# Kernel optimization log

Measured on AMD Instinct MI355X. Metric: run time of the kernel, lower is better.

Reference implementation:

```python
import jax, jax.numpy as jnp
import numpy as np

B, U, D_DEC, D_ENC = 32, 4096, 512, 512
ATT_UNITS, NUM_HEADS = 512, 4
HEAD_DIM = ATT_UNITS // NUM_HEADS
CONV_FILTERS, CONV_K = 32, 31
INIT = 0.075


def setup_inputs() -> dict:
    key = jax.random.key(0)
    ks = jax.random.split(key, 12)
    u = lambda k, shape: jax.random.uniform(k, shape, jnp.float32, -INIT, INIT)
    return {
        "dec_state": jax.random.normal(ks[0], (B, D_DEC), jnp.float32),
        "enc_state": jax.random.normal(ks[1], (B, U, D_ENC), jnp.float32),
        "prev_attention_weights": jax.random.uniform(ks[2], (B, U), jnp.float32),
        # stacked per-head Dense params
        "Wphi": u(ks[3], (NUM_HEADS, D_DEC, HEAD_DIM)),
        "bphi": jnp.zeros((NUM_HEADS, HEAD_DIM), jnp.float32),
        "Wpsi": u(ks[4], (NUM_HEADS, D_ENC, HEAD_DIM)),
        "bpsi": jnp.zeros((NUM_HEADS, HEAD_DIM), jnp.float32),
        # Conv1D kernel in WIO layout: (kernel_size, in_ch=1, out_ch=32), no bias
        "conv_kernel": jax.random.uniform(ks[5], (CONV_K, 1, CONV_FILTERS), jnp.float32, -0.1, 0.1),
        "Wloc": u(ks[6], (CONV_FILTERS, NUM_HEADS)),
        "Wout": u(ks[7], (NUM_HEADS * D_ENC, ATT_UNITS)),
        "bout": jnp.zeros((ATT_UNITS,), jnp.float32),
    }


def reference(dec_state, enc_state, prev_attention_weights,
              Wphi, bphi, Wpsi, bpsi, conv_kernel, Wloc, Wout, bout):
    # location features: Conv1D(same, no bias) over prev attention weights
    loc_feat = jax.lax.conv_general_dilated(
        prev_attention_weights[:, :, None], conv_kernel,
        window_strides=(1,), padding="SAME",
        dimension_numbers=("NWC", "WIO", "NWC"))            # (B, U, 32)
    loc_bias = loc_feat @ Wloc                                 # (B, U, H)
    loc_bias = jnp.transpose(loc_bias, (0, 2, 1))              # (B, H, U)

    # batched per-head projections (replaces the Python per-head loop)
    phi_s = jnp.einsum("bd,hdk->bhk", dec_state, Wphi) + bphi          # (B, H, hd)
    psi_h = jnp.einsum("bue,hek->bhuk", enc_state, Wpsi) + bpsi[:, None, :]  # (B, H, U, hd)

    energy = jnp.einsum("bhk,bhuk->bhu", phi_s, psi_h) + loc_bias      # (B, H, U)
    attn = jax.nn.softmax(energy, axis=-1)                              # (B, H, U)

    context = jnp.einsum("bhu,bue->bhe", attn, enc_state)               # (B, H, E)
    combined = context.reshape(context.shape[0], -1)                    # (B, H*E)
    context_vector = combined @ Wout + bout                             # (B, ATT_UNITS)
    attention_weights = jnp.mean(attn, axis=1)                          # (B, U)
    return context_vector, attention_weights
```

## Files before the change

kernel.cpp:

```cpp
#include <hip/hip_runtime.h>
#include <math.h>

#define B  32
#define U  4096
#define D  512
#define H  4
#define HD 128
#define CK 31
#define CF 32
#define AU 512

#define BPB    32
#define ROWS_W 32

static __device__ __forceinline__ float readlane_f(float v, int l) {
    return __int_as_float(__builtin_amdgcn_readlane(__float_as_int(v), l));
}

__global__ __launch_bounds__(256) void prep_kernel(
    const float* __restrict__ dec,
    const float* __restrict__ Wphi,
    const float* __restrict__ bphi,
    const float* __restrict__ Wpsi,
    const float* __restrict__ bpsi,
    const float* __restrict__ convk,
    const float* __restrict__ Wloc,
    float* __restrict__ ws_v,
    float* __restrict__ ws_const,
    float* __restrict__ ws_ck)
{
    __shared__ float decs[D];
    __shared__ float phis2[2][HD];
    __shared__ float phis[HD];
    const int b = blockIdx.x / H, h = blockIdx.x % H;
    const int tid = threadIdx.x;

    for (int i = tid; i < D; i += 256) decs[i] = dec[b * D + i];
    __syncthreads();

    {
        const int k = tid & 127, half = tid >> 7;
        const int d0 = half * 256;
        float acc = 0.f;
        const float* wp = Wphi + (size_t)h * D * HD + (size_t)d0 * HD + k;
        #pragma unroll 8
        for (int d = 0; d < 256; ++d) acc += decs[d0 + d] * wp[(size_t)d * HD];
        phis2[half][k] = acc;
    }
    __syncthreads();
    if (tid < HD) phis[tid] = phis2[0][tid] + phis2[1][tid] + bphi[h * HD + tid];
    __syncthreads();

    if (tid == 0) {
        float c = 0.f;
        for (int k = 0; k < HD; ++k) c += phis[k] * bpsi[h * HD + k];
        ws_const[b * H + h] = c;
    }

    for (int e = tid; e < D; e += 256) {
        const float* wq = Wpsi + ((size_t)h * D + e) * HD;
        float acc = 0.f;
        #pragma unroll 8
        for (int k = 0; k < HD; ++k) acc += wq[k] * phis[k];
        ws_v[((size_t)b * H + h) * D + e] = acc;
    }

    if (blockIdx.x == 0 && tid < CK * H) {
        int t = tid / H, hh = tid % H;
        float acc = 0.f;
        for (int f = 0; f < CF; ++f) acc += convk[t * CF + f] * Wloc[f * H + hh];
        ws_ck[t * H + hh] = acc;
    }
}

__global__ __launch_bounds__(256, 4) void fused_pass1(
    const float* __restrict__ enc,
    const float* __restrict__ prevw,
    const float* __restrict__ ws_v,
    const float* __restrict__ ws_const,
    const float* __restrict__ ws_ck,
    float* __restrict__ energy,
    float* __restrict__ pctx,
    float* __restrict__ pms)
{
    const int b    = blockIdx.y;
    const int blk  = blockIdx.x;
    const int tid  = threadIdx.x;
    const int lane = tid & 63;
    const int wave = tid >> 6;
    const int ubase = (blk * 4 + wave) * ROWS_W;

    __shared__ float lctx[4][H][D];
    __shared__ float lms[4][H][2];
    __shared__ float lalpha[H][4];

    float4 v0[H], v1[H];
    #pragma unroll
    for (int h = 0; h < H; ++h) {
        const float* vp = ws_v + ((size_t)b * H + h) * D + lane * 8;
        v0[h] = *(const float4*)vp;
        v1[h] = *(const float4*)(vp + 4);
    }
    float ckr[H] = {0.f, 0.f, 0.f, 0.f};
    if (lane < CK) {
        #pragma unroll
        for (int h = 0; h < H; ++h) ckr[h] = ws_ck[lane * H + h];
    }
    float ct[H];
    #pragma unroll
    for (int h = 0; h < H; ++h) ct[h] = ws_const[b * H + h];

    float w0;
    {
        const int gi = ubase - 15 + lane;
        w0 = (gi >= 0 && gi < U) ? prevw[b * U + gi] : 0.f;
    }

    float m0 = -3.402823466e38f, m1 = m0, m2 = m0, m3 = m0;
    float s0 = 0.f, s1 = 0.f, s2 = 0.f, s3 = 0.f;
    float4 z = {0.f, 0.f, 0.f, 0.f};
    float4 c00 = z, c01 = z, c10 = z, c11 = z, c20 = z, c21 = z, c30 = z, c31 = z;

    const bool b16 = (lane & 16) != 0;
    const bool b32 = (lane & 32) != 0;

    const float* encb = enc + ((size_t)b * U + ubase) * D + lane * 8;
    float4 e0 = *(const float4*)encb;
    float4 e1 = *(const float4*)(encb + 4);

    for (int r = 0; r < ROWS_W; ++r) {
        float4 n0, n1;
        if (r < ROWS_W - 1) {
            const float* nx = encb + (size_t)(r + 1) * D;
            n0 = *(const float4*)nx;
            n1 = *(const float4*)(nx + 4);
        }
        const int u = ubase + r;
        float pw = __int_as_float(
            __builtin_amdgcn_ds_bpermute((r + lane) << 2, __float_as_int(w0)));

        float p0 = pw * ckr[0]
            + e0.x*v0[0].x + e0.y*v0[0].y + e0.z*v0[0].z + e0.w*v0[0].w
            + e1.x*v1[0].x + e1.y*v1[0].y + e1.z*v1[0].z + e1.w*v1[0].w;
        float p1 = pw * ckr[1]
            + e0.x*v0[1].x + e0.y*v0[1].y + e0.z*v0[1].z + e0.w*v0[1].w
            + e1.x*v1[1].x + e1.y*v1[1].y + e1.z*v1[1].z + e1.w*v1[1].w;
        float p2 = pw * ckr[2]
            + e0.x*v0[2].x + e0.y*v0[2].y + e0.z*v0[2].z + e0.w*v0[2].w
            + e1.x*v1[2].x + e1.y*v1[2].y + e1.z*v1[2].z + e1.w*v1[2].w;
        float p3 = pw * ckr[3]
            + e0.x*v0[3].x + e0.y*v0[3].y + e0.z*v0[3].z + e0.w*v0[3].w
            + e1.x*v1[3].x + e1.y*v1[3].y + e1.z*v1[3].z + e1.w*v1[3].w;

        float keepA = b16 ? p1 : p0, sendA = b16 ? p0 : p1;
        float a  = keepA + __shfl_xor(sendA, 16);
        float keepB = b16 ? p3 : p2, sendB = b16 ? p2 : p3;
        float bb = keepB + __shfl_xor(sendB, 16);
        float keepC = b32 ? bb : a, sendC = b32 ? a : bb;
        float c = keepC + __shfl_xor(sendC, 32);
        c += __shfl_xor(c, 1);
        c += __shfl_xor(c, 2);
        c += __shfl_xor(c, 4);
        c += __shfl_xor(c, 8);
        float eh0 = readlane_f(c, 0)  + ct[0];
        float eh1 = readlane_f(c, 16) + ct[1];
        float eh2 = readlane_f(c, 32) + ct[2];
        float eh3 = readlane_f(c, 48) + ct[3];

        if (lane < H) {
            float ev = (lane == 0) ? eh0 : (lane == 1) ? eh1 : (lane == 2) ? eh2 : eh3;
            energy[((size_t)b * H + lane) * U + u] = ev;
        }

        float mn0 = fmaxf(m0, eh0), mn1 = fmaxf(m1, eh1);
        float mn2 = fmaxf(m2, eh2), mn3 = fmaxf(m3, eh3);
        if (mn0 > m0 || mn1 > m1 || mn2 > m2 || mn3 > m3) {
            float a0 = __expf(m0 - mn0), a1 = __expf(m1 - mn1);
            float a2 = __expf(m2 - mn2), a3 = __expf(m3 - mn3);
            s0 *= a0; s1 *= a1; s2 *= a2; s3 *= a3;
            c00.x*=a0; c00.y*=a0; c00.z*=a0; c00.w*=a0; c01.x*=a0; c01.y*=a0; c01.z*=a0; c01.w*=a0;
            c10.x*=a1; c10.y*=a1; c10.z*=a1; c10.w*=a1; c11.x*=a1; c11.y*=a1; c11.z*=a1; c11.w*=a1;
            c20.x*=a2; c20.y*=a2; c20.z*=a2; c20.w*=a2; c21.x*=a2; c21.y*=a2; c21.z*=a2; c21.w*=a2;
            c30.x*=a3; c30.y*=a3; c30.z*=a3; c30.w*=a3; c31.x*=a3; c31.y*=a3; c31.z*=a3; c31.w*=a3;
            m0 = mn0; m1 = mn1; m2 = mn2; m3 = mn3;
        }
        float w0e = __expf(eh0 - m0), w1e = __expf(eh1 - m1);
        float w2e = __expf(eh2 - m2), w3e = __expf(eh3 - m3);
        s0 += w0e; s1 += w1e; s2 += w2e; s3 += w3e;
        c00.x += w0e*e0.x; c00.y += w0e*e0.y; c00.z += w0e*e0.z; c00.w += w0e*e0.w;
        c01.x += w0e*e1.x; c01.y += w0e*e1.y; c01.z += w0e*e1.z; c01.w += w0e*e1.w;
        c10.x += w1e*e0.x; c10.y += w1e*e0.y; c10.z += w1e*e0.z; c10.w += w1e*e0.w;
        c11.x += w1e*e1.x; c11.y += w1e*e1.y; c11.z += w1e*e1.z; c11.w += w1e*e1.w;
        c20.x += w2e*e0.x; c20.y += w2e*e0.y; c20.z += w2e*e0.z; c20.w += w2e*e0.w;
        c21.x += w2e*e1.x; c21.y += w2e*e1.y; c21.z += w2e*e1.z; c21.w += w2e*e1.w;
        c30.x += w3e*e0.x; c30.y += w3e*e0.y; c30.z += w3e*e0.z; c30.w += w3e*e0.w;
        c31.x += w3e*e1.x; c31.y += w3e*e1.y; c31.z += w3e*e1.z; c31.w += w3e*e1.w;

        e0 = n0; e1 = n1;
    }

    *(float4*)&lctx[wave][0][lane * 8]     = c00;
    *(float4*)&lctx[wave][0][lane * 8 + 4] = c01;
    *(float4*)&lctx[wave][1][lane * 8]     = c10;
    *(float4*)&lctx[wave][1][lane * 8 + 4] = c11;
    *(float4*)&lctx[wave][2][lane * 8]     = c20;
    *(float4*)&lctx[wave][2][lane * 8 + 4] = c21;
    *(float4*)&lctx[wave][3][lane * 8]     = c30;
    *(float4*)&lctx[wave][3][lane * 8 + 4] = c31;
    if (lane == 0) {
        lms[wave][0][0] = m0; lms[wave][0][1] = s0;
        lms[wave][1][0] = m1; lms[wave][1][1] = s1;
        lms[wave][2][0] = m2; lms[wave][2][1] = s2;
        lms[wave][3][0] = m3; lms[wave][3][1] = s3;
    }
    __syncthreads();

    const size_t pbase = ((size_t)(b * BPB + blk)) * H;
    if (tid < H) {
        const int h = tid;
        float M = fmaxf(fmaxf(lms[0][h][0], lms[1][h][0]),
                        fmaxf(lms[2][h][0], lms[3][h][0]));
        float S = 0.f;
        #pragma unroll
        for (int w = 0; w < 4; ++w) {
            float al = __expf(lms[w][h][0] - M);
            lalpha[h][w] = al;
            S += al * lms[w][h][1];
        }
        pms[(pbase + h) * 2]     = M;
        pms[(pbase + h) * 2 + 1] = S;
    }
    __syncthreads();

    #pragma unroll
    for (int h = 0; h < H; ++h) {
        const float a0 = lalpha[h][0], a1 = lalpha[h][1];
        const float a2 = lalpha[h][2], a3 = lalpha[h][3];
        #pragma unroll
        for (int half = 0; half < 2; ++half) {
            const int d = tid + half * 256;
            float val = a0 * lctx[0][h][d] + a1 * lctx[1][h][d]
                      + a2 * lctx[2][h][d] + a3 * lctx[3][h][d];
            pctx[(pbase + h) * D + d] = val;
        }
    }
}

__global__ __launch_bounds__(256) void combine_kernel(
    const float* __restrict__ pctx,
    const float* __restrict__ pms,
    float* __restrict__ ctx,
    float* __restrict__ MS)
{
    const int bh = blockIdx.x;
    const int b = bh >> 2, h = bh & 3;
    const int tid = threadIdx.x;
    __shared__ float sm[BPB], ss[BPB], salpha[BPB];
    __shared__ float MSsh[2];

    if (tid < BPB) {
        sm[tid] = pms[(((size_t)b * BPB + tid) * H + h) * 2];
        ss[tid] = pms[(((size_t)b * BPB + tid) * H + h) * 2 + 1];
    }
    __syncthreads();
    if (tid == 0) {
        float M = -3.402823466e38f;
        for (int i = 0; i < BPB; ++i) M = fmaxf(M, sm[i]);
        float S = 0.f;
        for (int i = 0; i < BPB; ++i) {
            float al = __expf(sm[i] - M);
            salpha[i] = al;
            S += al * ss[i];
        }
        MSsh[0] = M; MSsh[1] = S;
        MS[bh * 2] = M; MS[bh * 2 + 1] = S;
    }
    __syncthreads();
    const float invS = 1.0f / MSsh[1];

    float acc0 = 0.f, acc1 = 0.f;
    const float* base = pctx + ((size_t)b * BPB * H + h) * D;
    #pragma unroll 4
    for (int i = 0; i < BPB; ++i) {
        float al = salpha[i];
        const float* p = base + (size_t)i * H * D;
        acc0 += al * p[tid];
        acc1 += al * p[tid + 256];
    }
    ctx[(size_t)bh * D + tid]       = acc0 * invS;
    ctx[(size_t)bh * D + tid + 256] = acc1 * invS;
}

__global__ __launch_bounds__(256) void attw_kernel(
    const float* __restrict__ energy,
    const float* __restrict__ MS,
    float* __restrict__ attw)
{
    const int b = blockIdx.x, tid = threadIdx.x;
    float M[H], iS[H];
    #pragma unroll
    for (int h = 0; h < H; ++h) {
        M[h]  = MS[(b * H + h) * 2];
        iS[h] = 1.0f / MS[(b * H + h) * 2 + 1];
    }
    #pragma unroll
    for (int i = 0; i < 16; ++i) {
        const int u = tid + i * 256;
        float acc = 0.f;
        #pragma unroll
        for (int h = 0; h < H; ++h)
            acc += __expf(energy[((size_t)b * H + h) * U + u] - M[h]) * iS[h];
        attw[(size_t)b * U + u] = acc * 0.25f;
    }
}

__global__ __launch_bounds__(256) void outproj_kernel(
    const float* __restrict__ ctx,
    const float* __restrict__ Wout,
    const float* __restrict__ bout,
    float* __restrict__ outv)
{
    const int b = blockIdx.y;
    const int j = blockIdx.x * 256 + threadIdx.x;
    const int i0 = blockIdx.z * 256;
    __shared__ float c_s[256];
    c_s[threadIdx.x] = ctx[(size_t)b * (H * D) + i0 + threadIdx.x];
    __syncthreads();

    float acc = (blockIdx.z == 0) ? bout[j] : 0.f;
    #pragma unroll 8
    for (int i = 0; i < 256; ++i)
        acc += c_s[i] * Wout[(size_t)(i0 + i) * AU + j];
    atomicAdd(&outv[(size_t)b * AU + j], acc);
}

extern "C" void kernel_launch(void* const* d_in, const int* in_sizes, int n_in,
                              void* d_out, int out_size, void* d_ws, size_t ws_size,
                              hipStream_t stream) {
    const float* dec   = (const float*)d_in[0];
    const float* enc   = (const float*)d_in[1];
    const float* prevw = (const float*)d_in[2];
    const float* Wphi  = (const float*)d_in[3];
    const float* bphi  = (const float*)d_in[4];
    const float* Wpsi  = (const float*)d_in[5];
    const float* bpsi  = (const float*)d_in[6];
    const float* convk = (const float*)d_in[7];
    const float* Wloc  = (const float*)d_in[8];
    const float* Wout  = (const float*)d_in[9];
    const float* bout  = (const float*)d_in[10];

    float* out  = (float*)d_out;
    float* outv = out;
    float* attw = out + B * AU;

    float* ws        = (float*)d_ws;
    float* ws_v      = ws;
    float* ws_const  = ws + 65536;
    float* ws_ck     = ws + 65664;
    float* ws_energy = ws + 65792;
    float* ws_pctx   = ws_energy + (size_t)B*H*U;
    float* ws_pms    = ws_pctx + (size_t)B*BPB*H*D;
    float* ws_MS     = ws_pms + (size_t)B*BPB*H*2;
    float* ws_ctx    = ws_MS + 256;

    hipMemsetAsync(outv, 0, (size_t)B * AU * sizeof(float), stream);

    prep_kernel<<<dim3(B * H), 256, 0, stream>>>(dec, Wphi, bphi, Wpsi, bpsi,
                                                 convk, Wloc, ws_v, ws_const, ws_ck);
    fused_pass1<<<dim3(BPB, B), 256, 0, stream>>>(enc, prevw, ws_v, ws_const,
                                                  ws_ck, ws_energy, ws_pctx, ws_pms);
    combine_kernel<<<dim3(B * H), 256, 0, stream>>>(ws_pctx, ws_pms, ws_ctx, ws_MS);
    attw_kernel<<<dim3(B), 256, 0, stream>>>(ws_energy, ws_MS, attw);
    outproj_kernel<<<dim3(2, B, 8), 256, 0, stream>>>(ws_ctx, Wout, bout, outv);
}
```

Baseline: 437.2 us.

## Deepen enc prefetch, batch energy stores per wave, widen attw grid

The fused pass now prefetches encoder rows two steps ahead instead of one and unrolls the row loop by two, so more memory latency is hidden. Energy values are collected in registers (lane r keeps row r) and written once after the loop as coalesced stores, replacing a scattered per-row store by four lanes. The attention-weight kernel grid grows from B to 8×B blocks, so many more CUs share the elementwise pass. These raise register pressure in the hot loop in exchange.

```diff
diff --git a/kernel.cpp b/kernel.cpp
--- a/kernel.cpp
+++ b/kernel.cpp
@@ -120,37 +120,40 @@
     float s0 = 0.f, s1 = 0.f, s2 = 0.f, s3 = 0.f;
     float4 z = {0.f, 0.f, 0.f, 0.f};
     float4 c00 = z, c01 = z, c10 = z, c11 = z, c20 = z, c21 = z, c30 = z, c31 = z;
+    float ea0 = 0.f, ea1 = 0.f, ea2 = 0.f, ea3 = 0.f;
 
     const bool b16 = (lane & 16) != 0;
     const bool b32 = (lane & 32) != 0;
 
     const float* encb = enc + ((size_t)b * U + ubase) * D + lane * 8;
-    float4 e0 = *(const float4*)encb;
-    float4 e1 = *(const float4*)(encb + 4);
-
+    float4 eA0 = *(const float4*)encb;
+    float4 eA1 = *(const float4*)(encb + 4);
+    float4 eB0 = *(const float4*)(encb + D);
+    float4 eB1 = *(const float4*)(encb + D + 4);
+
+    #pragma unroll 2
     for (int r = 0; r < ROWS_W; ++r) {
-        float4 n0, n1;
-        if (r < ROWS_W - 1) {
-            const float* nx = encb + (size_t)(r + 1) * D;
-            n0 = *(const float4*)nx;
-            n1 = *(const float4*)(nx + 4);
-        }
-        const int u = ubase + r;
+        float4 eC0, eC1;
+        if (r < ROWS_W - 2) {
+            const float* nx = encb + (size_t)(r + 2) * D;
+            eC0 = *(const float4*)nx;
+            eC1 = *(const float4*)(nx + 4);
+        }
         float pw = __int_as_float(
             __builtin_amdgcn_ds_bpermute((r + lane) << 2, __float_as_int(w0)));
 
         float p0 = pw * ckr[0]
-            + e0.x*v0[0].x + e0.y*v0[0].y + e0.z*v0[0].z + e0.w*v0[0].w
-            + e1.x*v1[0].x + e1.y*v1[0].y + e1.z*v1[0].z + e1.w*v1[0].w;
+            + eA0.x*v0[0].x + eA0.y*v0[0].y + eA0.z*v0[0].z + eA0.w*v0[0].w
+            + eA1.x*v1[0].x + eA1.y*v1[0].y + eA1.z*v1[0].z + eA1.w*v1[0].w;
         float p1 = pw * ckr[1]
-            + e0.x*v0[1].x + e0.y*v0[1].y + e0.z*v0[1].z + e0.w*v0[1].w
-            + e1.x*v1[1].x + e1.y*v1[1].y + e1.z*v1[1].z + e1.w*v1[1].w;
+            + eA0.x*v0[1].x + eA0.y*v0[1].y + eA0.z*v0[1].z + eA0.w*v0[1].w
+            + eA1.x*v1[1].x + eA1.y*v1[1].y + eA1.z*v1[1].z + eA1.w*v1[1].w;
         float p2 = pw * ckr[2]
-            + e0.x*v0[2].x + e0.y*v0[2].y + e0.z*v0[2].z + e0.w*v0[2].w
-            + e1.x*v1[2].x + e1.y*v1[2].y + e1.z*v1[2].z + e1.w*v1[2].w;
+            + eA0.x*v0[2].x + eA0.y*v0[2].y + eA0.z*v0[2].z + eA0.w*v0[2].w
+            + eA1.x*v1[2].x + eA1.y*v1[2].y + eA1.z*v1[2].z + eA1.w*v1[2].w;
         float p3 = pw * ckr[3]
-            + e0.x*v0[3].x + e0.y*v0[3].y + e0.z*v0[3].z + e0.w*v0[3].w
-            + e1.x*v1[3].x + e1.y*v1[3].y + e1.z*v1[3].z + e1.w*v1[3].w;
+            + eA0.x*v0[3].x + eA0.y*v0[3].y + eA0.z*v0[3].z + eA0.w*v0[3].w
+            + eA1.x*v1[3].x + eA1.y*v1[3].y + eA1.z*v1[3].z + eA1.w*v1[3].w;
 
         float keepA = b16 ? p1 : p0, sendA = b16 ? p0 : p1;
         float a  = keepA + __shfl_xor(sendA, 16);
@@ -167,10 +170,10 @@
         float eh2 = readlane_f(c, 32) + ct[2];
         float eh3 = readlane_f(c, 48) + ct[3];
 
-        if (lane < H) {
-            float ev = (lane == 0) ? eh0 : (lane == 1) ? eh1 : (lane == 2) ? eh2 : eh3;
-            energy[((size_t)b * H + lane) * U + u] = ev;
-        }
+        ea0 = (lane == r) ? eh0 : ea0;
+        ea1 = (lane == r) ? eh1 : ea1;
+        ea2 = (lane == r) ? eh2 : ea2;
+        ea3 = (lane == r) ? eh3 : ea3;
 
         float mn0 = fmaxf(m0, eh0), mn1 = fmaxf(m1, eh1);
         float mn2 = fmaxf(m2, eh2), mn3 = fmaxf(m3, eh3);
@@ -187,16 +190,25 @@
         float w0e = __expf(eh0 - m0), w1e = __expf(eh1 - m1);
         float w2e = __expf(eh2 - m2), w3e = __expf(eh3 - m3);
         s0 += w0e; s1 += w1e; s2 += w2e; s3 += w3e;
-        c00.x += w0e*e0.x; c00.y += w0e*e0.y; c00.z += w0e*e0.z; c00.w += w0e*e0.w;
-        c01.x += w0e*e1.x; c01.y += w0e*e1.y; c01.z += w0e*e1.z; c01.w += w0e*e1.w;
-        c10.x += w1e*e0.x; c10.y += w1e*e0.y; c10.z += w1e*e0.z; c10.w += w1e*e0.w;
-        c11.x += w1e*e1.x; c11.y += w1e*e1.y; c11.z += w1e*e1.z; c11.w += w1e*e1.w;
-        c20.x += w2e*e0.x; c20.y += w2e*e0.y; c20.z += w2e*e0.z; c20.w += w2e*e0.w;
-        c21.x += w2e*e1.x; c21.y += w2e*e1.y; c21.z += w2e*e1.z; c21.w += w2e*e1.w;
-        c30.x += w3e*e0.x; c30.y += w3e*e0.y; c30.z += w3e*e0.z; c30.w += w3e*e0.w;
-        c31.x += w3e*e1.x; c31.y += w3e*e1.y; c31.z += w3e*e1.z; c31.w += w3e*e1.w;
-
-        e0 = n0; e1 = n1;
+        c00.x += w0e*eA0.x; c00.y += w0e*eA0.y; c00.z += w0e*eA0.z; c00.w += w0e*eA0.w;
+        c01.x += w0e*eA1.x; c01.y += w0e*eA1.y; c01.z += w0e*eA1.z; c01.w += w0e*eA1.w;
+        c10.x += w1e*eA0.x; c10.y += w1e*eA0.y; c10.z += w1e*eA0.z; c10.w += w1e*eA0.w;
+        c11.x += w1e*eA1.x; c11.y += w1e*eA1.y; c11.z += w1e*eA1.z; c11.w += w1e*eA1.w;
+        c20.x += w2e*eA0.x; c20.y += w2e*eA0.y; c20.z += w2e*eA0.z; c20.w += w2e*eA0.w;
+        c21.x += w2e*eA1.x; c21.y += w2e*eA1.y; c21.z += w2e*eA1.z; c21.w += w2e*eA1.w;
+        c30.x += w3e*eA0.x; c30.y += w3e*eA0.y; c30.z += w3e*eA0.z; c30.w += w3e*eA0.w;
+        c31.x += w3e*eA1.x; c31.y += w3e*eA1.y; c31.z += w3e*eA1.z; c31.w += w3e*eA1.w;
+
+        eA0 = eB0; eA1 = eB1;
+        eB0 = eC0; eB1 = eC1;
+    }
+
+    if (lane < ROWS_W) {
+        const int u = ubase + lane;
+        energy[((size_t)b * H + 0) * U + u] = ea0;
+        energy[((size_t)b * H + 1) * U + u] = ea1;
+        energy[((size_t)b * H + 2) * U + u] = ea2;
+        energy[((size_t)b * H + 3) * U + u] = ea3;
     }
 
     *(float4*)&lctx[wave][0][lane * 8]     = c00;
@@ -296,7 +308,8 @@
     const float* __restrict__ MS,
     float* __restrict__ attw)
 {
-    const int b = blockIdx.x, tid = threadIdx.x;
+    const int b = blockIdx.y, tid = threadIdx.x;
+    const int u0 = blockIdx.x * 512;
     float M[H], iS[H];
     #pragma unroll
     for (int h = 0; h < H; ++h) {
@@ -304,8 +317,8 @@
         iS[h] = 1.0f / MS[(b * H + h) * 2 + 1];
     }
     #pragma unroll
-    for (int i = 0; i < 16; ++i) {
-        const int u = tid + i * 256;
+    for (int i = 0; i < 2; ++i) {
+        const int u = u0 + tid + i * 256;
         float acc = 0.f;
         #pragma unroll
         for (int h = 0; h < H; ++h)
@@ -370,6 +383,6 @@
     fused_pass1<<<dim3(BPB, B), 256, 0, stream>>>(enc, prevw, ws_v, ws_const,
                                                   ws_ck, ws_energy, ws_pctx, ws_pms);
     combine_kernel<<<dim3(B * H), 256, 0, stream>>>(ws_pctx, ws_pms, ws_ctx, ws_MS);
-    attw_kernel<<<dim3(B), 256, 0, stream>>>(ws_energy, ws_MS, attw);
+    attw_kernel<<<dim3(8, B), 256, 0, stream>>>(ws_energy, ws_MS, attw);
     outproj_kernel<<<dim3(2, B, 8), 256, 0, stream>>>(ws_ctx, Wout, bout, outv);
 }
```

Measured after the change: 455.9 us. +4.3%, slower.
